# Kernel optimization log

Hardware: AMD Instinct MI355X
Metric: run time of the kernel (lower is better)

The kernel has to match this reference:

```python
import jax, jax.numpy as jnp
import numpy as np

EPS = 1e-8  # torch.cosine_similarity default eps


def _gelu(x):
    # torch nn.GELU default = exact (erf) gelu
    return jax.nn.gelu(x, approximate=False)


def setup_inputs() -> dict:
    key = jax.random.key(0)
    ks = jax.random.split(key, 12)
    B, D, H1, E, N, K = 32768, 768, 256, 128, 500, 5
    TOT = D + E + 1 + 1 + 4  # 902, importance_net input dim
    s = 0.02
    return {
        "cue": jax.random.normal(ks[0], (B, D), jnp.float32),
        "internal_state": jnp.zeros((B, E), jnp.float32),
        "reward": jax.random.uniform(ks[1], (B, 1), dtype=jnp.float32),
        "timestamp": jax.random.uniform(ks[2], (B, 1), dtype=jnp.float32),
        "emotional_state": jax.random.uniform(ks[3], (B, 4), dtype=jnp.float32),
        "centroids": jax.random.normal(ks[4], (N, E), jnp.float32),
        "enc_w1": jax.random.normal(ks[5], (D, H1), jnp.float32) * s,
        "enc_b1": jnp.zeros((H1,), jnp.float32),
        "enc_w2": jax.random.normal(ks[6], (H1, E), jnp.float32) * s,
        "enc_b2": jnp.zeros((E,), jnp.float32),
        "imp_w1": jax.random.normal(ks[7], (TOT, 64), jnp.float32) * s,
        "imp_b1": jnp.zeros((64,), jnp.float32),
        "imp_w2": jax.random.normal(ks[8], (64, 1), jnp.float32) * s,
        "imp_b2": jnp.zeros((1,), jnp.float32),
        "top_k": K,
    }


def reference(cue, internal_state, reward, timestamp, emotional_state, centroids,
              enc_w1, enc_b1, enc_w2, enc_b2,
              imp_w1, imp_b1, imp_w2, imp_b2, top_k):
    # --- encoder MLP (batched over all cues instead of per-item calls) ---
    enc = _gelu(cue @ enc_w1 + enc_b1) @ enc_w2 + enc_b2        # [B, 128]

    # --- cosine similarity vs all cluster centroids (fused loop) ---
    num = enc @ centroids.T                                      # [B, N]
    e_n = jnp.linalg.norm(enc, axis=-1, keepdims=True)           # [B, 1]
    c_n = jnp.linalg.norm(centroids, axis=-1)                    # [N]
    sims = num / jnp.maximum(e_n * c_n[None, :], EPS)            # [B, N]
    top_vals, _ = jax.lax.top_k(sims, top_k)                     # [B, K]

    # --- importance net on combined memory entry ---
    combined = jnp.concatenate(
        [cue, internal_state, reward, timestamp, emotional_state], axis=-1)  # [B, 902]
    imp = jax.nn.sigmoid(_gelu(combined @ imp_w1 + imp_b1) @ imp_w2 + imp_b2)  # [B, 1]
    imp = imp * jnp.mean(emotional_state, axis=-1, keepdims=True)

    return jnp.concatenate([top_vals, imp], axis=-1)             # [B, K+1]
```

## Files before the change

kernel.cpp:

```cpp
#include <hip/hip_runtime.h>
#include <hip/hip_bf16.h>
#include <hip/hip_fp16.h>
#include <math.h>

using f32x4  = __attribute__((ext_vector_type(4))) float;
using half8  = __attribute__((ext_vector_type(8))) _Float16;
using uint4v = __attribute__((ext_vector_type(4))) unsigned int;

#define WAITV(N) asm volatile("s_waitcnt vmcnt(" #N ")" ::: "memory")
#define LGKM0    asm volatile("s_waitcnt lgkmcnt(0)" ::: "memory")

__device__ __forceinline__ unsigned short f32_to_f16u(float f) {
  return __half_as_ushort(__float2half(f));
}
__device__ __forceinline__ float f16u_to_f32(unsigned short h) {
  return __half2float(__ushort_as_half(h));
}
__device__ __forceinline__ unsigned int pk2(float a, float b) {
  return (unsigned int)f32_to_f16u(a) | ((unsigned int)f32_to_f16u(b) << 16);
}
__device__ __forceinline__ f32x4 mfma16(half8 a, half8 b, f32x4 c) {
  return __builtin_amdgcn_mfma_f32_16x16x32_f16(a, b, c, 0, 0, 0);
}
__device__ __forceinline__ void gload_lds16(void* lds, const void* g) {
  __builtin_amdgcn_global_load_lds(
      (const __attribute__((address_space(1))) unsigned int*)g,
      (__attribute__((address_space(3))) unsigned int*)lds, 16, 0, 0);
}
__device__ __forceinline__ float gelu_exact(float x) {
  return 0.5f * x * (1.0f + erff(x * 0.70710678118654752440f));
}


__global__ __launch_bounds__(256) void k_prep(
    const float* __restrict__ enc_w1, const float* __restrict__ enc_w2,
    const float* __restrict__ imp_w1, const float* __restrict__ cent,
    const float* __restrict__ reward, const float* __restrict__ tsp,
    const float* __restrict__ emo,
    unsigned short* __restrict__ W1T, unsigned short* __restrict__ W2T,
    unsigned short* __restrict__ impW1T, unsigned short* __restrict__ centC,
    float* __restrict__ c_n, unsigned short* __restrict__ tail) {
  __shared__ float ld[64][65];
  const int bx = blockIdx.x, t = threadIdx.x;
  if (bx < 48) {
    int tk = bx % 12, tn = bx / 12;
    int k0 = tk * 64, n0 = tn * 64;
    int cn = t & 63, r4 = t >> 6;
#pragma unroll
    for (int pass = 0; pass < 16; ++pass) {
      int kk = pass * 4 + r4;
      ld[kk][cn] = enc_w1[(size_t)(k0 + kk) * 256 + n0 + cn];
    }
    __syncthreads();
    int ck = t & 63, rn4 = t >> 6;
#pragma unroll
    for (int pass = 0; pass < 16; ++pass) {
      int nn = pass * 4 + rn4;
      W1T[(size_t)(n0 + nn) * 768 + k0 + ck] = f32_to_f16u(ld[ck][nn]);
    }
    return;
  }
  int idx = (bx - 48) * 256 + t;
  if (idx < 128 * 256) {
    int n = idx >> 8, k = idx & 255;
    W2T[idx] = f32_to_f16u(enc_w2[k * 128 + n]);
  }
  if (idx < 64 * 960) {
    int n = idx / 960, k = idx - n * 960;
    impW1T[idx] = (k < 902) ? f32_to_f16u(imp_w1[k * 64 + n]) : (unsigned short)0;
  }
  if (idx < 512 * 128) {
    int n = idx >> 7, k = idx & 127;
    centC[idx] = (n < 500) ? f32_to_f16u(cent[n * 128 + k]) : (unsigned short)0;
  }
  if (idx < 512) {
    float s = 0.f;
    if (idx < 500) {
      const f32x4* p = (const f32x4*)(cent + idx * 128);
#pragma unroll 8
      for (int j = 0; j < 32; ++j) {
        f32x4 v = p[j];
#pragma unroll
        for (int e = 0; e < 4; ++e) {
          float q = (float)(_Float16)v[e];
          s += q * q;
        }
      }
    }
    c_n[idx] = sqrtf(s);
  }
  if (idx < 32768) {
    f32x4 e4 = *(const f32x4*)(emo + (size_t)idx * 4);
    unsigned short* tp = tail + (size_t)idx * 8;
    tp[0] = f32_to_f16u(reward[idx]);
    tp[1] = f32_to_f16u(tsp[idx]);
    tp[2] = f32_to_f16u(e4[0]); tp[3] = f32_to_f16u(e4[1]);
    tp[4] = f32_to_f16u(e4[2]); tp[5] = f32_to_f16u(e4[3]);
    tp[6] = 0; tp[7] = 0;
  }
}

__global__ __launch_bounds__(512, 4) void k_encimp(
    const float* __restrict__ cue, const float* __restrict__ internal,
    const float* __restrict__ emo,
    const unsigned short* __restrict__ W1T, const unsigned short* __restrict__ impW1T,
    const unsigned short* __restrict__ tail,
    const float* __restrict__ b1, const float* __restrict__ ib1,
    const float* __restrict__ iw2, const float* __restrict__ ib2,
    unsigned short* __restrict__ h1, float* __restrict__ out) {
  __shared__ unsigned char sm[73728];
  const int t = threadIdx.x;
  const int lane = t & 63, w = t >> 6;
  const int wr = w >> 2, wc = w & 3;
  const int g = lane >> 4, c = lane & 15;
  const int row0 = blockIdx.x * 64;

  const int srow = t >> 3, q8 = t & 7;
  const int abyte = srow * 128 + q8 * 16;
  const int aswz = (srow & 7) << 4;
  const int myrow = row0 + srow;

  f32x4 aLo, aHi;
  auto issueA = [&](int j) {
    const float* s = (j < 12)
        ? (cue + (size_t)myrow * 768 + j * 64 + q8 * 8)
        : (internal + (size_t)myrow * 128 + (j - 12) * 64 + q8 * 8);
    aLo = *(const f32x4*)s;
    aHi = *(const f32x4*)(s + 4);
  };
  auto convWrite = [&](int buf) {
    uint4v u = {pk2(aLo[0], aLo[1]), pk2(aLo[2], aLo[3]),
                pk2(aHi[0], aHi[1]), pk2(aHi[2], aHi[3])};
    *(uint4v*)(sm + buf * 8192 + (abyte ^ aswz)) = u;
  };
  auto issueB1 = [&](int j) {
#pragma unroll
    for (int i = 0; i < 4; ++i) {
      int L = i * 8192 + t * 16;
      int nl = L >> 7, x = L & 127;
      gload_lds16(sm + 24576 + i * 8192 + w * 1024,
                  (const unsigned char*)W1T + ((size_t)nl * 768 + j * 64) * 2 +
                      (x ^ ((nl & 7) << 4)));
    }
  };
  auto issueB2 = [&](int j, int buf) {
    int L = t * 16, nl = L >> 7, x = L & 127;
    gload_lds16(sm + 57344 + buf * 8192 + w * 1024,
                (const unsigned char*)impW1T + (size_t)nl * 1920 + j * 128 +
                    (x ^ ((nl & 7) << 4)));
  };

  f32x4 acc1[2][4];
  f32x4 acc2[2];
#pragma unroll
  for (int i = 0; i < 2; ++i) {
    acc2[i] = f32x4{0.f, 0.f, 0.f, 0.f};
#pragma unroll
    for (int j = 0; j < 4; ++j) acc1[i][j] = f32x4{0.f, 0.f, 0.f, 0.f};
  }

  auto mfma_step = [&](int abuf, int b2buf, bool enc) {
    const unsigned char* Ab  = sm + abuf * 8192;
    const unsigned char* Bb2 = sm + 57344 + b2buf * 8192;
#pragma unroll
    for (int ks = 0; ks < 2; ++ks) {
      half8 af[2];
#pragma unroll
      for (int mf = 0; mf < 2; ++mf) {
        int m = wr * 32 + mf * 16 + c;
        af[mf] = *(const half8*)(Ab + m * 128 + ((ks * 64 + g * 16) ^ ((m & 7) << 4)));
      }
      {
        int n2 = wc * 16 + c;
        half8 b2f = *(const half8*)(Bb2 + n2 * 128 + ((ks * 64 + g * 16) ^ ((n2 & 7) << 4)));
        acc2[0] = mfma16(af[0], b2f, acc2[0]);
        acc2[1] = mfma16(af[1], b2f, acc2[1]);
      }
      if (enc) {
#pragma unroll
        for (int nf = 0; nf < 4; ++nf) {
          int n = wc * 64 + nf * 16 + c;
          half8 bf = *(const half8*)(sm + 24576 + n * 128 +
                                     ((ks * 64 + g * 16) ^ ((n & 7) << 4)));
          acc1[0][nf] = mfma16(af[0], bf, acc1[0][nf]);
          acc1[1][nf] = mfma16(af[1], bf, acc1[1][nf]);
        }
      }
    }
  };

  {
    uint4v tl = {0u, 0u, 0u, 0u};
    if (q8 == 0) tl = *(const uint4v*)(tail + (size_t)myrow * 8);
    issueA(0); issueB1(0); issueB2(0, 0);
    *(uint4v*)(sm + 16384 + (abyte ^ aswz)) = tl;
    convWrite(0);
    issueA(1); issueB2(1, 1);
    WAITV(3);
    LGKM0;
    __builtin_amdgcn_s_barrier();
  }

  int p = 0;
  for (int it = 0; it < 12; ++it) {
    mfma_step(p, p, true);
    convWrite(p ^ 1);
    LGKM0;
    __builtin_amdgcn_s_barrier();
    if (it < 11) issueB1(it + 1);
    issueA(it + 2);
    issueB2(it + 2, p);
    WAITV(3);
    __builtin_amdgcn_s_barrier();
    p ^= 1;
  }
  mfma_step(0, 0, false);
  convWrite(1);
  LGKM0;
  __builtin_amdgcn_s_barrier();
  issueB2(14, 0);
  WAITV(1);
  __builtin_amdgcn_s_barrier();
  mfma_step(1, 1, false);
  LGKM0;
  __builtin_amdgcn_s_barrier();
  WAITV(0);
  __builtin_amdgcn_s_barrier();
  mfma_step(2, 0, false);

  float bias1[4];
#pragma unroll
  for (int nf = 0; nf < 4; ++nf) bias1[nf] = b1[wc * 64 + nf * 16 + c];
#pragma unroll
  for (int mf = 0; mf < 2; ++mf)
#pragma unroll
    for (int nf = 0; nf < 4; ++nf)
#pragma unroll
      for (int rr = 0; rr < 4; ++rr) {
        float x = acc1[mf][nf][rr] + bias1[nf];
        int m = row0 + wr * 32 + mf * 16 + g * 4 + rr;
        int n = wc * 64 + nf * 16 + c;
        h1[(size_t)m * 256 + n] = f32_to_f16u(gelu_exact(x));
      }

  {
    float* s_p = (float*)(sm + 24576);
    float b1v = ib1[wc * 16 + c];
    float w2v = iw2[wc * 16 + c];
#pragma unroll
    for (int mf = 0; mf < 2; ++mf)
#pragma unroll
      for (int rr = 0; rr < 4; ++rr) {
        float v = gelu_exact(acc2[mf][rr] + b1v) * w2v;
        v += __shfl_xor(v, 1);
        v += __shfl_xor(v, 2);
        v += __shfl_xor(v, 4);
        v += __shfl_xor(v, 8);
        if (c == 0) s_p[(wr * 32 + mf * 16 + g * 4 + rr) * 4 + wc] = v;
      }
    __syncthreads();
    if (t < 64) {
      float ssum = s_p[t * 4 + 0] + s_p[t * 4 + 1] + s_p[t * 4 + 2] + s_p[t * 4 + 3];
      int rowA = row0 + t;
      float z = ssum + ib2[0];
      float sig = 1.0f / (1.0f + expf(-z));
      f32x4 e4 = *(const f32x4*)(emo + (size_t)rowA * 4);
      float m4 = 0.25f * (e4[0] + e4[1] + e4[2] + e4[3]);
      out[(size_t)rowA * 6 + 5] = sig * m4;
    }
  }
}

__global__ __launch_bounds__(256) void k_tail(
    const unsigned short* __restrict__ h1, const unsigned short* __restrict__ W2T,
    const unsigned short* __restrict__ centC, const float* __restrict__ c_n,
    const float* __restrict__ b2, unsigned short* __restrict__ enc,
    float* __restrict__ out) {
  __shared__ unsigned char smA[32768];
  __shared__ unsigned char smB[32768];
  __shared__ float s_pn[256];
  __shared__ float s_en[64];
  const int t = threadIdx.x, lane = t & 63, w = t >> 6;
  const int g = lane >> 4, c = lane & 15;
  const int row0 = blockIdx.x * 64;

#pragma unroll
  for (int i = 0; i < 8; ++i) {
    int L = i * 4096 + t * 16;
    int rl = L >> 9, x = L & 511;
    gload_lds16(smA + i * 4096 + w * 1024,
                (const unsigned char*)h1 + (size_t)(row0 + rl) * 512 +
                    (x ^ ((rl & 7) << 4)));
  }

  float nsq[4][4];
#pragma unroll
  for (int mf = 0; mf < 4; ++mf)
#pragma unroll
    for (int rr = 0; rr < 4; ++rr) nsq[mf][rr] = 0.f;

  for (int h = 0; h < 2; ++h) {
#pragma unroll
    for (int i = 0; i < 8; ++i) {
      int L = i * 4096 + t * 16;
      int nl = L >> 9, x = L & 511;
      gload_lds16(smB + i * 4096 + w * 1024,
                  (const unsigned char*)W2T + (size_t)(h * 64 + nl) * 512 +
                      (x ^ ((nl & 7) << 4)));
    }
    __syncthreads();

    f32x4 acc_e[4];
#pragma unroll
    for (int mf = 0; mf < 4; ++mf) acc_e[mf] = f32x4{0.f, 0.f, 0.f, 0.f};
#pragma unroll
    for (int ks = 0; ks < 8; ++ks) {
      half8 af[4];
#pragma unroll
      for (int mf = 0; mf < 4; ++mf) {
        int rl = mf * 16 + c;
        af[mf] = *(const half8*)(smA + rl * 512 +
                                 ((ks * 64 + g * 16) ^ ((rl & 7) << 4)));
      }
      int nl = w * 16 + c;
      half8 bf = *(const half8*)(smB + nl * 512 +
                                 ((ks * 64 + g * 16) ^ ((nl & 7) << 4)));
#pragma unroll
      for (int mf = 0; mf < 4; ++mf) acc_e[mf] = mfma16(af[mf], bf, acc_e[mf]);
    }
    float bias = b2[h * 64 + w * 16 + c];
#pragma unroll
    for (int mf = 0; mf < 4; ++mf)
#pragma unroll
      for (int rr = 0; rr < 4; ++rr) {
        float x = acc_e[mf][rr] + bias;
        unsigned short hv = f32_to_f16u(x);
        float xr = f16u_to_f32(hv);
        nsq[mf][rr] += xr * xr;
        int m = row0 + mf * 16 + g * 4 + rr;
        enc[(size_t)m * 128 + h * 64 + w * 16 + c] = hv;
      }
    __syncthreads();
  }

#pragma unroll
  for (int mf = 0; mf < 4; ++mf)
#pragma unroll
    for (int rr = 0; rr < 4; ++rr) {
      float v = nsq[mf][rr];
      v += __shfl_xor(v, 1);
      v += __shfl_xor(v, 2);
      v += __shfl_xor(v, 4);
      v += __shfl_xor(v, 8);
      if (c == 0) s_pn[(mf * 16 + g * 4 + rr) * 4 + w] = v;
    }
  WAITV(0);
  __syncthreads();
  if (t < 64)
    s_en[t] = sqrtf(s_pn[t * 4 + 0] + s_pn[t * 4 + 1] +
                    s_pn[t * 4 + 2] + s_pn[t * 4 + 3]);
  __syncthreads();

  float en[4];
#pragma unroll
  for (int r = 0; r < 4; ++r) en[r] = s_en[w * 16 + g * 4 + r];

  half8 af2[4];
  {
    const unsigned char* abase =
        (const unsigned char*)enc + (size_t)(row0 + w * 16 + c) * 256 + g * 16;
#pragma unroll
    for (int kk = 0; kk < 4; ++kk) af2[kk] = *(const half8*)(abase + kk * 64);
  }

  unsigned int top5[4][5];
#pragma unroll
  for (int r = 0; r < 4; ++r)
#pragma unroll
    for (int s5 = 0; s5 < 5; ++s5) top5[r][s5] = 0u;

#pragma unroll
  for (int ch = 0; ch < 4; ++ch) {
    __syncthreads();
#pragma unroll
    for (int i = 0; i < 8; ++i) {
      int L = i * 4096 + t * 16;
      int nl = L >> 8, x = L & 255;
      const unsigned char* gs = (const unsigned char*)centC +
          (size_t)(ch * 128 + nl) * 256 + (x ^ ((nl & 7) << 4));
      gload_lds16(smB + i * 4096 + w * 1024, gs);
    }
    __syncthreads();

    f32x4 acc[8];
#pragma unroll
    for (int i = 0; i < 8; ++i) acc[i] = f32x4{0.f, 0.f, 0.f, 0.f};
#pragma unroll
    for (int nfc = 0; nfc < 8; ++nfc) {
      int nl = nfc * 16 + c;
      const unsigned char* bbase = smB + nl * 256;
      int swz = (nl & 7) << 4;
#pragma unroll
      for (int kk = 0; kk < 4; ++kk) {
        half8 bf = *(const half8*)(bbase + ((kk * 64 + g * 16) ^ swz));
        acc[nfc] = mfma16(af2[kk], bf, acc[nfc]);
      }
    }

#pragma unroll
    for (int nfc = 0; nfc < 8; ++nfc) {
      int col = ch * 128 + nfc * 16 + c;
      float cnv = c_n[col];
#pragma unroll
      for (int r = 0; r < 4; ++r) {
        float denom = fmaxf(en[r] * cnv, 1e-8f);
        float v = acc[nfc][r] * __builtin_amdgcn_rcpf(denom);
        unsigned int u = __float_as_uint(v);
        u = (u & 0x80000000u) ? ~u : (u | 0x80000000u);
        unsigned int k = (col < 500) ? ((u & 0xFFFFFE00u) | (unsigned)col) : 0u;
        unsigned int t0 = top5[r][0], t1 = top5[r][1], t2 = top5[r][2],
                     t3 = top5[r][3], t4 = top5[r][4];
        top5[r][0] = (k > t0) ? k : t0;
        top5[r][1] = (k > t0) ? t0 : ((k > t1) ? k : t1);
        top5[r][2] = (k > t1) ? t1 : ((k > t2) ? k : t2);
        top5[r][3] = (k > t2) ? t2 : ((k > t3) ? k : t3);
        top5[r][4] = (k > t3) ? t3 : ((k > t4) ? k : t4);
      }
    }
  }

#pragma unroll
  for (int r = 0; r < 4; ++r) {
    int rowA = row0 + w * 16 + g * 4 + r;
    unsigned int h0 = top5[r][0], h1v = top5[r][1], h2 = top5[r][2],
                 h3 = top5[r][3], h4 = top5[r][4];
#pragma unroll
    for (int it5 = 0; it5 < 5; ++it5) {
      unsigned int best = h0;
#pragma unroll
      for (int s = 1; s < 16; s <<= 1) {
        unsigned int o = __shfl_xor(best, s);
        best = (o > best) ? o : best;
      }
      if (c == 0) {
        unsigned int m = best & 0xFFFFFE00u;
        unsigned int uu = (m & 0x80000000u) ? (m ^ 0x80000000u) : ~m;
        out[(size_t)rowA * 6 + it5] = __uint_as_float(uu);
      }
      bool pop = (h0 == best);
      h0 = pop ? h1v : h0;
      h1v = pop ? h2 : h1v;
      h2 = pop ? h3 : h2;
      h3 = pop ? h4 : h3;
      h4 = pop ? 0u : h4;
    }
  }
}

extern "C" void kernel_launch(void* const* d_in, const int* in_sizes, int n_in,
                              void* d_out, int out_size, void* d_ws, size_t ws_size,
                              hipStream_t stream) {
  (void)in_sizes; (void)n_in; (void)out_size; (void)ws_size;
  const float* cue      = (const float*)d_in[0];
  const float* internal = (const float*)d_in[1];
  const float* reward   = (const float*)d_in[2];
  const float* tsp      = (const float*)d_in[3];
  const float* emo      = (const float*)d_in[4];
  const float* cent     = (const float*)d_in[5];
  const float* enc_w1   = (const float*)d_in[6];
  const float* enc_b1   = (const float*)d_in[7];
  const float* enc_w2   = (const float*)d_in[8];
  const float* enc_b2   = (const float*)d_in[9];
  const float* imp_w1   = (const float*)d_in[10];
  const float* imp_b1   = (const float*)d_in[11];
  const float* imp_w2   = (const float*)d_in[12];
  const float* imp_b2   = (const float*)d_in[13];
  float* out = (float*)d_out;

  unsigned char* ws = (unsigned char*)d_ws;
  unsigned short* h1     = (unsigned short*)(ws + 0);
  unsigned short* enc    = (unsigned short*)(ws + 16777216);
  unsigned short* W1T    = (unsigned short*)(ws + 25165824);
  unsigned short* W2T    = (unsigned short*)(ws + 25559040);
  unsigned short* impW1T = (unsigned short*)(ws + 25624576);
  unsigned short* centC  = (unsigned short*)(ws + 25747456);
  float*          c_n    = (float*)(ws + 25878528);
  unsigned short* tail   = (unsigned short*)(ws + 25880576);

  k_prep<<<304, 256, 0, stream>>>(enc_w1, enc_w2, imp_w1, cent, reward, tsp, emo,
                                  W1T, W2T, impW1T, centC, c_n, tail);
  k_encimp<<<512, 512, 0, stream>>>(cue, internal, emo, W1T, impW1T, tail,
                                    enc_b1, imp_b1, imp_w2, imp_b2, h1, out);
  k_tail<<<512, 256, 0, stream>>>(h1, W2T, centC, c_n, enc_b2, enc, out);
}
```

Measured before the change: 72.19 us.

## Fuse encoder second layer and centroid top-k into the encoder/importance kernel

Merges the tail kernel into the first GEMM kernel. The GELU hidden activations and the encoder output now stay in shared memory instead of going through global scratch buffers, which removes a 16MB write and read of h1, the enc round-trip and one launch. The centroid top-5 work is split across two halves of the 8 waves, and the per-half top-5 lists are merged at the end. In exchange the larger kernel may carry more register and LDS pressure and hold more barriers.

```diff
diff --git a/kernel.cpp b/kernel.cpp
--- a/kernel.cpp
+++ b/kernel.cpp
@@ -100,14 +100,16 @@
   }
 }
 
-__global__ __launch_bounds__(512, 4) void k_encimp(
+__global__ __launch_bounds__(512, 4) void k_fused(
     const float* __restrict__ cue, const float* __restrict__ internal,
     const float* __restrict__ emo,
     const unsigned short* __restrict__ W1T, const unsigned short* __restrict__ impW1T,
     const unsigned short* __restrict__ tail,
-    const float* __restrict__ b1, const float* __restrict__ ib1,
-    const float* __restrict__ iw2, const float* __restrict__ ib2,
-    unsigned short* __restrict__ h1, float* __restrict__ out) {
+    const unsigned short* __restrict__ W2T, const unsigned short* __restrict__ centC,
+    const float* __restrict__ c_n,
+    const float* __restrict__ b1, const float* __restrict__ b2,
+    const float* __restrict__ ib1, const float* __restrict__ iw2,
+    const float* __restrict__ ib2, float* __restrict__ out) {
   __shared__ unsigned char sm[73728];
   const int t = threadIdx.x;
   const int lane = t & 63, w = t >> 6;
@@ -228,23 +230,14 @@
   __builtin_amdgcn_s_barrier();
   mfma_step(2, 0, false);
 
-  float bias1[4];
-#pragma unroll
-  for (int nf = 0; nf < 4; ++nf) bias1[nf] = b1[wc * 64 + nf * 16 + c];
-#pragma unroll
-  for (int mf = 0; mf < 2; ++mf)
-#pragma unroll
-    for (int nf = 0; nf < 4; ++nf)
-#pragma unroll
-      for (int rr = 0; rr < 4; ++rr) {
-        float x = acc1[mf][nf][rr] + bias1[nf];
-        int m = row0 + wr * 32 + mf * 16 + g * 4 + rr;
-        int n = wc * 64 + nf * 16 + c;
-        h1[(size_t)m * 256 + n] = f32_to_f16u(gelu_exact(x));
-      }
+  float* s_pn = (float*)(sm + 65536);
+  float* s_en = (float*)(sm + 67584);
+  float* s_p  = (float*)(sm + 67840);
+  unsigned int* s_mk = (unsigned int*)(sm + 68864);
+
+  __syncthreads();
 
   {
-    float* s_p = (float*)(sm + 24576);
     float b1v = ib1[wc * 16 + c];
     float w2v = iw2[wc * 16 + c];
 #pragma unroll
@@ -258,119 +251,106 @@
         v += __shfl_xor(v, 8);
         if (c == 0) s_p[(wr * 32 + mf * 16 + g * 4 + rr) * 4 + wc] = v;
       }
+    float bias1[4];
+#pragma unroll
+    for (int nf = 0; nf < 4; ++nf) bias1[nf] = b1[wc * 64 + nf * 16 + c];
+#pragma unroll
+    for (int mf = 0; mf < 2; ++mf)
+#pragma unroll
+      for (int nf = 0; nf < 4; ++nf)
+#pragma unroll
+        for (int rr = 0; rr < 4; ++rr) {
+          int row = wr * 32 + mf * 16 + g * 4 + rr;
+          int col = wc * 64 + nf * 16 + c;
+          float x = gelu_exact(acc1[mf][nf][rr] + bias1[nf]);
+          *(unsigned short*)(sm + row * 512 + ((col * 2) ^ ((row & 7) << 4))) =
+              f32_to_f16u(x);
+        }
+  }
+  __syncthreads();
+
+  if (t < 64) {
+    float ssum = s_p[t * 4 + 0] + s_p[t * 4 + 1] + s_p[t * 4 + 2] + s_p[t * 4 + 3];
+    int rowA = row0 + t;
+    float z = ssum + ib2[0];
+    float sig = 1.0f / (1.0f + expf(-z));
+    f32x4 e4 = *(const f32x4*)(emo + (size_t)rowA * 4);
+    float m4 = 0.25f * (e4[0] + e4[1] + e4[2] + e4[3]);
+    out[(size_t)rowA * 6 + 5] = sig * m4;
+  }
+
+  f32x4 acc_e[4];
+#pragma unroll
+  for (int mf = 0; mf < 4; ++mf) acc_e[mf] = f32x4{0.f, 0.f, 0.f, 0.f};
+#pragma unroll
+  for (int kh = 0; kh < 2; ++kh) {
+#pragma unroll
+    for (int i = 0; i < 4; ++i) {
+      int L = i * 8192 + t * 16;
+      int nl = L >> 8, x = L & 255;
+      gload_lds16(sm + 32768 + i * 8192 + w * 1024,
+                  (const unsigned char*)W2T + (size_t)nl * 512 + kh * 256 +
+                      (x ^ ((nl & 7) << 4)));
+    }
     __syncthreads();
-    if (t < 64) {
-      float ssum = s_p[t * 4 + 0] + s_p[t * 4 + 1] + s_p[t * 4 + 2] + s_p[t * 4 + 3];
-      int rowA = row0 + t;
-      float z = ssum + ib2[0];
-      float sig = 1.0f / (1.0f + expf(-z));
-      f32x4 e4 = *(const f32x4*)(emo + (size_t)rowA * 4);
-      float m4 = 0.25f * (e4[0] + e4[1] + e4[2] + e4[3]);
-      out[(size_t)rowA * 6 + 5] = sig * m4;
-    }
-  }
-}
-
-__global__ __launch_bounds__(256) void k_tail(
-    const unsigned short* __restrict__ h1, const unsigned short* __restrict__ W2T,
-    const unsigned short* __restrict__ centC, const float* __restrict__ c_n,
-    const float* __restrict__ b2, unsigned short* __restrict__ enc,
-    float* __restrict__ out) {
-  __shared__ unsigned char smA[32768];
-  __shared__ unsigned char smB[32768];
-  __shared__ float s_pn[256];
-  __shared__ float s_en[64];
-  const int t = threadIdx.x, lane = t & 63, w = t >> 6;
-  const int g = lane >> 4, c = lane & 15;
-  const int row0 = blockIdx.x * 64;
-
-#pragma unroll
-  for (int i = 0; i < 8; ++i) {
-    int L = i * 4096 + t * 16;
-    int rl = L >> 9, x = L & 511;
-    gload_lds16(smA + i * 4096 + w * 1024,
-                (const unsigned char*)h1 + (size_t)(row0 + rl) * 512 +
-                    (x ^ ((rl & 7) << 4)));
-  }
-
-  float nsq[4][4];
-#pragma unroll
-  for (int mf = 0; mf < 4; ++mf)
-#pragma unroll
-    for (int rr = 0; rr < 4; ++rr) nsq[mf][rr] = 0.f;
-
-  for (int h = 0; h < 2; ++h) {
-#pragma unroll
-    for (int i = 0; i < 8; ++i) {
-      int L = i * 4096 + t * 16;
-      int nl = L >> 9, x = L & 511;
-      gload_lds16(smB + i * 4096 + w * 1024,
-                  (const unsigned char*)W2T + (size_t)(h * 64 + nl) * 512 +
-                      (x ^ ((nl & 7) << 4)));
+#pragma unroll
+    for (int ks = 0; ks < 4; ++ks) {
+      half8 af[4];
+#pragma unroll
+      for (int mf = 0; mf < 4; ++mf) {
+        int m = mf * 16 + c;
+        af[mf] = *(const half8*)(sm + m * 512 +
+                                 ((kh * 256 + ks * 64 + g * 16) ^ ((m & 7) << 4)));
+      }
+      int nl = w * 16 + c;
+      half8 bf = *(const half8*)(sm + 32768 + nl * 256 +
+                                 ((ks * 64 + g * 16) ^ ((nl & 7) << 4)));
+#pragma unroll
+      for (int mf = 0; mf < 4; ++mf) acc_e[mf] = mfma16(af[mf], bf, acc_e[mf]);
     }
     __syncthreads();
-
-    f32x4 acc_e[4];
-#pragma unroll
-    for (int mf = 0; mf < 4; ++mf) acc_e[mf] = f32x4{0.f, 0.f, 0.f, 0.f};
-#pragma unroll
-    for (int ks = 0; ks < 8; ++ks) {
-      half8 af[4];
-#pragma unroll
-      for (int mf = 0; mf < 4; ++mf) {
-        int rl = mf * 16 + c;
-        af[mf] = *(const half8*)(smA + rl * 512 +
-                                 ((ks * 64 + g * 16) ^ ((rl & 7) << 4)));
-      }
-      int nl = w * 16 + c;
-      half8 bf = *(const half8*)(smB + nl * 512 +
-                                 ((ks * 64 + g * 16) ^ ((nl & 7) << 4)));
-#pragma unroll
-      for (int mf = 0; mf < 4; ++mf) acc_e[mf] = mfma16(af[mf], bf, acc_e[mf]);
-    }
-    float bias = b2[h * 64 + w * 16 + c];
+  }
+
+  {
+    float bias2 = b2[w * 16 + c];
 #pragma unroll
     for (int mf = 0; mf < 4; ++mf)
 #pragma unroll
       for (int rr = 0; rr < 4; ++rr) {
-        float x = acc_e[mf][rr] + bias;
+        int row = mf * 16 + g * 4 + rr;
+        float x = acc_e[mf][rr] + bias2;
         unsigned short hv = f32_to_f16u(x);
         float xr = f16u_to_f32(hv);
-        nsq[mf][rr] += xr * xr;
-        int m = row0 + mf * 16 + g * 4 + rr;
-        enc[(size_t)m * 128 + h * 64 + w * 16 + c] = hv;
-      }
-    __syncthreads();
-  }
-
-#pragma unroll
-  for (int mf = 0; mf < 4; ++mf)
-#pragma unroll
-    for (int rr = 0; rr < 4; ++rr) {
-      float v = nsq[mf][rr];
-      v += __shfl_xor(v, 1);
-      v += __shfl_xor(v, 2);
-      v += __shfl_xor(v, 4);
-      v += __shfl_xor(v, 8);
-      if (c == 0) s_pn[(mf * 16 + g * 4 + rr) * 4 + w] = v;
-    }
-  WAITV(0);
+        *(unsigned short*)(sm + row * 256 + (((w * 16 + c) * 2) ^ ((row & 7) << 4))) = hv;
+        float v = xr * xr;
+        v += __shfl_xor(v, 1);
+        v += __shfl_xor(v, 2);
+        v += __shfl_xor(v, 4);
+        v += __shfl_xor(v, 8);
+        if (c == 0) s_pn[row * 8 + w] = v;
+      }
+  }
   __syncthreads();
-  if (t < 64)
-    s_en[t] = sqrtf(s_pn[t * 4 + 0] + s_pn[t * 4 + 1] +
-                    s_pn[t * 4 + 2] + s_pn[t * 4 + 3]);
+  if (t < 64) {
+    float s = 0.f;
+#pragma unroll
+    for (int i = 0; i < 8; ++i) s += s_pn[t * 8 + i];
+    s_en[t] = sqrtf(s);
+  }
   __syncthreads();
 
+  const int rlb = (w & 3) * 16;
+  const int halfsel = w >> 2;
   float en[4];
 #pragma unroll
-  for (int r = 0; r < 4; ++r) en[r] = s_en[w * 16 + g * 4 + r];
-
+  for (int r = 0; r < 4; ++r) en[r] = s_en[rlb + g * 4 + r];
   half8 af2[4];
   {
-    const unsigned char* abase =
-        (const unsigned char*)enc + (size_t)(row0 + w * 16 + c) * 256 + g * 16;
-#pragma unroll
-    for (int kk = 0; kk < 4; ++kk) af2[kk] = *(const half8*)(abase + kk * 64);
+    int rl = rlb + c;
+#pragma unroll
+    for (int kk = 0; kk < 4; ++kk)
+      af2[kk] = *(const half8*)(sm + rl * 256 +
+                                ((kk * 64 + g * 16) ^ ((rl & 7) << 4)));
   }
 
   unsigned int top5[4][5];
@@ -383,38 +363,31 @@
   for (int ch = 0; ch < 4; ++ch) {
     __syncthreads();
 #pragma unroll
-    for (int i = 0; i < 8; ++i) {
-      int L = i * 4096 + t * 16;
+    for (int i = 0; i < 4; ++i) {
+      int L = i * 8192 + t * 16;
       int nl = L >> 8, x = L & 255;
-      const unsigned char* gs = (const unsigned char*)centC +
-          (size_t)(ch * 128 + nl) * 256 + (x ^ ((nl & 7) << 4));
-      gload_lds16(smB + i * 4096 + w * 1024, gs);
+      gload_lds16(sm + 32768 + i * 8192 + w * 1024,
+                  (const unsigned char*)centC + (size_t)(ch * 128 + nl) * 256 +
+                      (x ^ ((nl & 7) << 4)));
     }
     __syncthreads();
-
-    f32x4 acc[8];
-#pragma unroll
-    for (int i = 0; i < 8; ++i) acc[i] = f32x4{0.f, 0.f, 0.f, 0.f};
-#pragma unroll
-    for (int nfc = 0; nfc < 8; ++nfc) {
-      int nl = nfc * 16 + c;
-      const unsigned char* bbase = smB + nl * 256;
+#pragma unroll
+    for (int nfc = 0; nfc < 4; ++nfc) {
+      int nl = halfsel * 64 + nfc * 16 + c;
+      const unsigned char* bbase = sm + 32768 + nl * 256;
       int swz = (nl & 7) << 4;
+      f32x4 acc = f32x4{0.f, 0.f, 0.f, 0.f};
 #pragma unroll
       for (int kk = 0; kk < 4; ++kk) {
         half8 bf = *(const half8*)(bbase + ((kk * 64 + g * 16) ^ swz));
-        acc[nfc] = mfma16(af2[kk], bf, acc[nfc]);
-      }
-    }
-
-#pragma unroll
-    for (int nfc = 0; nfc < 8; ++nfc) {
-      int col = ch * 128 + nfc * 16 + c;
+        acc = mfma16(af2[kk], bf, acc);
+      }
+      int col = ch * 128 + nl;
       float cnv = c_n[col];
 #pragma unroll
       for (int r = 0; r < 4; ++r) {
         float denom = fmaxf(en[r] * cnv, 1e-8f);
-        float v = acc[nfc][r] * __builtin_amdgcn_rcpf(denom);
+        float v = acc[r] * __builtin_amdgcn_rcpf(denom);
         unsigned int u = __float_as_uint(v);
         u = (u & 0x80000000u) ? ~u : (u | 0x80000000u);
         unsigned int k = (col < 500) ? ((u & 0xFFFFFE00u) | (unsigned)col) : 0u;
@@ -431,7 +404,7 @@
 
 #pragma unroll
   for (int r = 0; r < 4; ++r) {
-    int rowA = row0 + w * 16 + g * 4 + r;
+    int row = rlb + g * 4 + r;
     unsigned int h0 = top5[r][0], h1v = top5[r][1], h2 = top5[r][2],
                  h3 = top5[r][3], h4 = top5[r][4];
 #pragma unroll
@@ -442,17 +415,30 @@
         unsigned int o = __shfl_xor(best, s);
         best = (o > best) ? o : best;
       }
-      if (c == 0) {
-        unsigned int m = best & 0xFFFFFE00u;
-        unsigned int uu = (m & 0x80000000u) ? (m ^ 0x80000000u) : ~m;
-        out[(size_t)rowA * 6 + it5] = __uint_as_float(uu);
-      }
+      if (c == 0) s_mk[(row * 2 + halfsel) * 5 + it5] = best;
       bool pop = (h0 == best);
       h0 = pop ? h1v : h0;
       h1v = pop ? h2 : h1v;
       h2 = pop ? h3 : h2;
       h3 = pop ? h4 : h3;
       h4 = pop ? 0u : h4;
+    }
+  }
+  __syncthreads();
+
+  if (t < 64) {
+    const unsigned int* A = s_mk + (t * 2 + 0) * 5;
+    const unsigned int* B = s_mk + (t * 2 + 1) * 5;
+    int ia = 0, ib = 0;
+#pragma unroll
+    for (int o = 0; o < 5; ++o) {
+      unsigned int a = (ia < 5) ? A[ia] : 0u;
+      unsigned int b = (ib < 5) ? B[ib] : 0u;
+      unsigned int best;
+      if (a >= b) { best = a; ++ia; } else { best = b; ++ib; }
+      unsigned int m = best & 0xFFFFFE00u;
+      unsigned int uu = (m & 0x80000000u) ? (m ^ 0x80000000u) : ~m;
+      out[(size_t)(row0 + t) * 6 + o] = __uint_as_float(uu);
     }
   }
 }
@@ -478,18 +464,16 @@
   float* out = (float*)d_out;
 
   unsigned char* ws = (unsigned char*)d_ws;
-  unsigned short* h1     = (unsigned short*)(ws + 0);
-  unsigned short* enc    = (unsigned short*)(ws + 16777216);
-  unsigned short* W1T    = (unsigned short*)(ws + 25165824);
-  unsigned short* W2T    = (unsigned short*)(ws + 25559040);
-  unsigned short* impW1T = (unsigned short*)(ws + 25624576);
-  unsigned short* centC  = (unsigned short*)(ws + 25747456);
-  float*          c_n    = (float*)(ws + 25878528);
-  unsigned short* tail   = (unsigned short*)(ws + 25880576);
+  unsigned short* W1T    = (unsigned short*)(ws + 0);
+  unsigned short* W2T    = (unsigned short*)(ws + 393216);
+  unsigned short* impW1T = (unsigned short*)(ws + 458752);
+  unsigned short* centC  = (unsigned short*)(ws + 581632);
+  float*          c_n    = (float*)(ws + 712704);
+  unsigned short* tail   = (unsigned short*)(ws + 714752);
 
   k_prep<<<304, 256, 0, stream>>>(enc_w1, enc_w2, imp_w1, cent, reward, tsp, emo,
                                   W1T, W2T, impW1T, centC, c_n, tail);
-  k_encimp<<<512, 512, 0, stream>>>(cue, internal, emo, W1T, impW1T, tail,
-                                    enc_b1, imp_b1, imp_w2, imp_b2, h1, out);
-  k_tail<<<512, 256, 0, stream>>>(h1, W2T, centC, c_n, enc_b2, enc, out);
-}
+  k_fused<<<512, 512, 0, stream>>>(cue, internal, emo, W1T, impW1T, tail,
+                                   W2T, centC, c_n, enc_b1, enc_b2,
+                                   imp_b1, imp_w2, imp_b2, out);
+}
```

Measured after the change: 63.13 us (median of 3 runs). 1.14x faster.
